# Kernel tuning notes

Measured on AMD Instinct MI355X. Metric: run time of the kernel, lower is better.

The kernel has to match this reference:

```python
import jax, jax.numpy as jnp
import numpy as np

N, E = 10000, 160000
RNA, PROT, EMB, HID, H = 2000, 100, 128, 128, 4
D_IN = 2 * EMB          # 256, input to last block
D_MID = HID * 4         # 512, after conv1/lin1 residual (heads*channel)


def _gat(x, src, dst, Ws, Wd, att_s, att_d, bias, n_nodes, heads):
    # PyG GATConv (tuple in_channels -> separate src/dst linears, concat=True,
    # add_self_loops=False, negative_slope=0.2, eval mode so dropout is identity)
    C = Ws.shape[1] // heads
    xs = (x @ Ws).reshape(n_nodes, heads, C)   # [N,H,C]
    xd = (x @ Wd).reshape(n_nodes, heads, C)
    a_s = jnp.sum(xs * att_s, axis=-1)          # [N,H]
    a_d = jnp.sum(xd * att_d, axis=-1)
    alpha = jax.nn.leaky_relu(a_s[src] + a_d[dst], 0.2)   # [E,H]
    m = jax.ops.segment_max(alpha, dst, num_segments=n_nodes)  # [N,H]
    alpha = jnp.exp(alpha - m[dst])
    denom = jax.ops.segment_sum(alpha, dst, num_segments=n_nodes)
    alpha = alpha / (denom[dst] + 1e-16)
    out = jax.ops.segment_sum(xs[src] * alpha[:, :, None], dst, num_segments=n_nodes)
    return out.reshape(n_nodes, heads * C) + bias


def _layernorm(h, g, b, eps=1e-5):
    mu = jnp.mean(h, axis=-1, keepdims=True)
    var = jnp.mean(jnp.square(h - mu), axis=-1, keepdims=True)
    return (h - mu) * jax.lax.rsqrt(var + eps) * g + b


def setup_inputs() -> dict:
    key = jax.random.key(0)
    ks = iter(jax.random.split(key, 40))
    w = lambda *s: jax.random.normal(next(ks), s, jnp.float32) * 0.02
    z = lambda *s: jnp.zeros(s, jnp.float32)
    inp = {}
    inp["x"] = jax.random.normal(next(ks), (N, RNA + PROT), jnp.float32)
    inp["edge_index"] = jax.random.randint(next(ks), (2, E), 0, N, jnp.int64)
    inp["W_rna"], inp["b_rna"] = w(RNA, EMB), z(EMB)
    inp["W_prot"], inp["b_prot"] = w(PROT, EMB), z(EMB)
    # last GraphAttnBlock (hidden_dim -> hidden_dim), the only one whose output is used
    inp["c1_Ws"], inp["c1_Wd"] = w(D_IN, H * HID), w(D_IN, H * HID)
    inp["c1_as"], inp["c1_ad"] = w(H, HID), w(H, HID)
    inp["c1_b"] = z(H * HID)
    inp["l1_W"], inp["l1_b"] = w(D_IN, D_MID), z(D_MID)
    inp["ln_g"], inp["ln_b"] = jnp.ones((D_MID,), jnp.float32), z(D_MID)
    inp["c2_Ws"], inp["c2_Wd"] = w(D_MID, H * HID), w(D_MID, H * HID)
    inp["c2_as"], inp["c2_ad"] = w(H, HID), w(H, HID)
    inp["c2_b"] = z(H * HID)
    inp["l2_W"], inp["l2_b"] = w(D_MID, D_MID), z(D_MID)
    inp["agg_W"], inp["agg_b"] = w(D_MID, HID), z(HID)
    inp["dr_W"], inp["dr_b"] = w(HID, EMB), z(EMB)
    inp["dp_W"], inp["dp_b"] = w(HID, EMB), z(EMB)
    inp["rr_W"], inp["rr_b"] = w(EMB, RNA), z(RNA)
    inp["rp_W"], inp["rp_b"] = w(EMB, PROT), z(PROT)
    return inp


def reference(x, edge_index, W_rna, b_rna, W_prot, b_prot,
              c1_Ws, c1_Wd, c1_as, c1_ad, c1_b, l1_W, l1_b, ln_g, ln_b,
              c2_Ws, c2_Wd, c2_as, c2_ad, c2_b, l2_W, l2_b,
              agg_W, agg_b, dr_W, dr_b, dp_W, dp_b, rr_W, rr_b, rp_W, rp_b):
    src, dst = edge_index[0], edge_index[1]
    rna_e = x[:, :RNA] @ W_rna + b_rna
    prot_e = x[:, RNA:] @ W_prot + b_prot
    xin = jnp.concatenate([rna_e, prot_e], axis=1)   # raw_x_input [N, 2*EMB]
    # source loops blocks over raw_x_input; only last block output survives
    h = _gat(xin, src, dst, c1_Ws, c1_Wd, c1_as, c1_ad, c1_b, N, H) + (xin @ l1_W + l1_b)
    h = jax.nn.relu(_layernorm(h, ln_g, ln_b))
    h = _gat(h, src, dst, c2_Ws, c2_Wd, c2_as, c2_ad, c2_b, N, H) + (h @ l2_W + l2_b)
    emb = jax.nn.relu(h @ agg_W + agg_b)
    rna_recon = (emb @ dr_W + dr_b) @ rr_W + rr_b
    prot_recon = (emb @ dp_W + dp_b) @ rp_W + rp_b
    return (rna_recon, prot_recon, emb)
```

## Files before the change

### kernel.cpp

```cpp
#include <hip/hip_runtime.h>
#include <hip/hip_bf16.h>
#include <stdint.h>
#include <stddef.h>

using bf16  = __hip_bfloat16;
using bf162 = __hip_bfloat162;

typedef __bf16 bvec8 __attribute__((ext_vector_type(8)));
typedef float  fvec4 __attribute__((ext_vector_type(4)));

struct __align__(16) bf16x8 { bf162 a, b, c, d; };

__device__ __forceinline__ void bf8_to_f(const bf16* p, float* o) {
    bf16x8 v = *reinterpret_cast<const bf16x8*>(p);
    o[0] = __bfloat162float(v.a.x); o[1] = __bfloat162float(v.a.y);
    o[2] = __bfloat162float(v.b.x); o[3] = __bfloat162float(v.b.y);
    o[4] = __bfloat162float(v.c.x); o[5] = __bfloat162float(v.c.y);
    o[6] = __bfloat162float(v.d.x); o[7] = __bfloat162float(v.d.y);
}

__device__ __forceinline__ float wred_sum(float v) {
    #pragma unroll
    for (int o = 32; o > 0; o >>= 1) v += __shfl_xor(v, o);
    return v;
}

__device__ __forceinline__ float wred_max(float v) {
    #pragma unroll
    for (int o = 32; o > 0; o >>= 1) v = fmaxf(v, __shfl_xor(v, o));
    return v;
}

__device__ __forceinline__ float lrelu(float x) { return (x > 0.f) ? x : 0.2f * x; }

__device__ __forceinline__ fvec4 mfma16(bvec8 a, bvec8 b, fvec4 c) {
    return __builtin_amdgcn_mfma_f32_16x16x32_bf16(a, b, c, 0, 0, 0);
}

__device__ __forceinline__ bvec8 ldA(const bf16* p) {
    return *reinterpret_cast<const bvec8*>(p);
}
__device__ __forceinline__ bvec8 ldA(const float* p) {
    float4 f0 = *reinterpret_cast<const float4*>(p);
    float4 f1 = *reinterpret_cast<const float4*>(p + 4);
    union { bvec8 v; bf16 h[8]; } u;
    u.h[0] = __float2bfloat16(f0.x); u.h[1] = __float2bfloat16(f0.y);
    u.h[2] = __float2bfloat16(f0.z); u.h[3] = __float2bfloat16(f0.w);
    u.h[4] = __float2bfloat16(f1.x); u.h[5] = __float2bfloat16(f1.y);
    u.h[6] = __float2bfloat16(f1.z); u.h[7] = __float2bfloat16(f1.w);
    return u.v;
}

__global__ void detect_kernel(const int* __restrict__ ei, int E, int* __restrict__ flags) {
    __shared__ int zc;
    if (threadIdx.x == 0) zc = 0;
    __syncthreads();
    int nodd = E / 2; if (nodd > 1024) nodd = 1024;
    for (int i = threadIdx.x; i < nodd; i += blockDim.x)
        if (ei[2 * i + 1] == 0) atomicAdd(&zc, 1);
    __syncthreads();
    if (threadIdx.x == 0) flags[0] = (zc > nodd / 2) ? 1 : 0;
}

__global__ void conv_edges_kernel(const int* __restrict__ ei, int* __restrict__ src32,
                                  int* __restrict__ dst32, int E, int N,
                                  const int* __restrict__ flags) {
    const int e = blockIdx.x * blockDim.x + threadIdx.x;
    if (e >= E) return;
    int s, d;
    if (flags[0]) { s = ei[2 * e]; d = ei[2 * (E + e)]; }
    else          { s = ei[e];     d = ei[E + e]; }
    src32[e] = (s < 0) ? 0 : ((s >= N) ? N - 1 : s);
    dst32[e] = (d < 0) ? 0 : ((d >= N) ? N - 1 : d);
}

__global__ void zero_int_kernel(int* __restrict__ p, int n) {
    int i = blockIdx.x * blockDim.x + threadIdx.x;
    if (i < n) p[i] = 0;
}

__global__ void hist_kernel(const int* __restrict__ dst32, int* __restrict__ cnt, int E) {
    int e = blockIdx.x * blockDim.x + threadIdx.x;
    if (e < E) atomicAdd(&cnt[dst32[e]], 1);
}

__global__ void scan_kernel(const int* __restrict__ cnt, int* __restrict__ row_ptr, int N) {
    __shared__ int sh[256];
    __shared__ int carry;
    if (threadIdx.x == 0) { carry = 0; row_ptr[0] = 0; }
    __syncthreads();
    for (int base = 0; base < N; base += 256) {
        int i = base + threadIdx.x;
        int v = (i < N) ? cnt[i] : 0;
        sh[threadIdx.x] = v;
        __syncthreads();
        #pragma unroll
        for (int o = 1; o < 256; o <<= 1) {
            int t = (threadIdx.x >= o) ? sh[threadIdx.x - o] : 0;
            __syncthreads();
            sh[threadIdx.x] += t;
            __syncthreads();
        }
        if (i < N) row_ptr[i + 1] = sh[threadIdx.x] + carry;
        __syncthreads();
        if (threadIdx.x == 0) carry += sh[255];
        __syncthreads();
    }
}

__global__ void fill_csr_kernel(const int* __restrict__ src32, const int* __restrict__ dst32,
                                const int* __restrict__ row_ptr, int* __restrict__ cursor,
                                int* __restrict__ col_src, int E) {
    int e = blockIdx.x * blockDim.x + threadIdx.x;
    if (e >= E) return;
    int d = dst32[e];
    int pos = atomicAdd(&cursor[d], 1);
    col_src[row_ptr[d] + pos] = src32[e];
}

__global__ __launch_bounds__(256) void conv_xprot_kernel(const float* __restrict__ x,
                                                         bf16* __restrict__ xp, int N) {
    int idx = blockIdx.x * blockDim.x + threadIdx.x;
    if (idx >= N * 128) return;
    int r = idx >> 7, c = idx & 127;
    float v = (c < 100) ? x[(size_t)r * 2100 + 2000 + c] : 0.f;
    xp[idx] = __float2bfloat16(v);
}

struct WEnt { const float* src; bf16* dst; int K, N, Kp, Np, start; };
struct WTab { WEnt e[12]; int n; };

__global__ __launch_bounds__(256) void wconv_all_kernel(WTab tab) {
    const int b = blockIdx.x;
    int wi = 0;
    #pragma unroll 1
    for (int i = 1; i < tab.n; ++i) if (b >= tab.e[i].start) wi = i;
    const WEnt w = tab.e[wi];
    const int t = (b - w.start) * 256 + threadIdx.x;
    if (t >= w.Np * w.Kp) return;
    const int n = t / w.Kp, k = t - n * w.Kp;
    float v = (n < w.N && k < w.K) ? w.src[(size_t)k * w.N + n] : 0.f;
    w.dst[t] = __float2bfloat16(v);
}

__global__ void bias_fuse_kernel(const float* l1_b, const float* c1_b, float* bsum1,
                                 const float* l2_b, const float* c2_b, float* bsum2,
                                 const float* dr_b, const float* dp_b, float* ddb) {
    int i = blockIdx.x * blockDim.x + threadIdx.x;
    if (i < 512)       bsum1[i] = l1_b[i] + c1_b[i];
    else if (i < 1024) bsum2[i - 512] = l2_b[i - 512] + c2_b[i - 512];
    else if (i < 1152) ddb[i - 1024] = dr_b[i - 1024];
    else if (i < 1280) ddb[i - 1024] = dp_b[i - 1152];
}

template <int FM, bool RELU, typename AT>
__global__ __launch_bounds__(256) void mfma_gemm_kernel(
    const AT* __restrict__ A, int lda,
    const bf16* __restrict__ Bt, int ldb,
    const float* __restrict__ bias,
    float* __restrict__ Cf, int ldcf,
    bf16* __restrict__ Cb, int ldcb,
    int M, int Nn, int K)
{
    const int tid  = threadIdx.x;
    const int w    = tid >> 6, lane = tid & 63;
    const int wr   = w >> 1,   wc   = w & 1;
    const int m0   = blockIdx.y * (FM * 32) + wr * (FM * 16);
    const int n0   = blockIdx.x * 64 + wc * 32;
    const int lrow = lane & 15;
    const int lk8  = (lane >> 4) * 8;

    const AT* Ap[FM];
    #pragma unroll
    for (int i = 0; i < FM; ++i) {
        int r = m0 + i * 16 + lrow;
        if (r > M - 1) r = M - 1;
        Ap[i] = A + (size_t)r * lda + lk8;
    }
    const bf16* Bp = Bt + (size_t)(n0 + lrow) * ldb + lk8;
    const size_t b16 = (size_t)16 * ldb;

    fvec4 acc[FM][2];
    const fvec4 z = {0.f, 0.f, 0.f, 0.f};
    #pragma unroll
    for (int i = 0; i < FM; ++i) { acc[i][0] = z; acc[i][1] = z; }

    #pragma unroll 2
    for (int k = 0; k < K; k += 32) {
        bvec8 b0 = *reinterpret_cast<const bvec8*>(Bp + k);
        bvec8 b1 = *reinterpret_cast<const bvec8*>(Bp + k + b16);
        #pragma unroll
        for (int i = 0; i < FM; ++i) {
            bvec8 a = ldA(Ap[i] + k);
            acc[i][0] = mfma16(a, b0, acc[i][0]);
            acc[i][1] = mfma16(a, b1, acc[i][1]);
        }
    }

    const int r4 = (lane >> 4) * 4;
    #pragma unroll
    for (int fn = 0; fn < 2; ++fn) {
        const int col = n0 + fn * 16 + lrow;
        if (col >= Nn) continue;
        const float bz = bias ? bias[col] : 0.f;
        #pragma unroll
        for (int fm = 0; fm < FM; ++fm) {
            const int rbase = m0 + fm * 16 + r4;
            #pragma unroll
            for (int r = 0; r < 4; ++r) {
                const int row = rbase + r;
                if (row >= M) continue;
                float v = acc[fm][fn][r] + bz;
                if (RELU) v = fmaxf(v, 0.f);
                if (Cf) Cf[(size_t)row * ldcf + col] = v;
                if (Cb) Cb[(size_t)row * ldcb + col] = __float2bfloat16(v);
            }
        }
    }
}

__global__ __launch_bounds__(256) void mfma_gemm_dual_kernel(
    const bf16* __restrict__ A, int lda,
    const bf16* __restrict__ Bt, int ldb,
    const float* __restrict__ biasU,
    bf16* __restrict__ xs, float* __restrict__ hB,
    int M, int K)
{
    const int tid  = threadIdx.x;
    const int w    = tid >> 6, lane = tid & 63;
    const int wr   = w >> 1,   wc   = w & 1;
    const int m0   = blockIdx.y * 128 + wr * 64;
    const int n0   = blockIdx.x * 64 + wc * 32;
    const int lrow = lane & 15;
    const int lk8  = (lane >> 4) * 8;

    const bf16* Ap[4];
    #pragma unroll
    for (int i = 0; i < 4; ++i) {
        int r = m0 + i * 16 + lrow;
        if (r > M - 1) r = M - 1;
        Ap[i] = A + (size_t)r * lda + lk8;
    }
    const bf16* Bp = Bt + (size_t)(n0 + lrow) * ldb + lk8;
    const size_t b16 = (size_t)16 * ldb;

    fvec4 acc[4][2];
    const fvec4 z = {0.f, 0.f, 0.f, 0.f};
    #pragma unroll
    for (int i = 0; i < 4; ++i) { acc[i][0] = z; acc[i][1] = z; }

    #pragma unroll 2
    for (int k = 0; k < K; k += 32) {
        bvec8 b0 = *reinterpret_cast<const bvec8*>(Bp + k);
        bvec8 b1 = *reinterpret_cast<const bvec8*>(Bp + k + b16);
        #pragma unroll
        for (int i = 0; i < 4; ++i) {
            bvec8 a = *reinterpret_cast<const bvec8*>(Ap[i] + k);
            acc[i][0] = mfma16(a, b0, acc[i][0]);
            acc[i][1] = mfma16(a, b1, acc[i][1]);
        }
    }

    const int r4 = (lane >> 4) * 4;
    #pragma unroll
    for (int fn = 0; fn < 2; ++fn) {
        const int col = n0 + fn * 16 + lrow;
        if (col < 512) {
            #pragma unroll
            for (int fm = 0; fm < 4; ++fm) {
                const int rbase = m0 + fm * 16 + r4;
                #pragma unroll
                for (int r = 0; r < 4; ++r) {
                    const int row = rbase + r;
                    if (row >= M) continue;
                    xs[(size_t)row * 512 + col] = __float2bfloat16(acc[fm][fn][r]);
                }
            }
        } else {
            const int c2 = col - 512;
            const float bz = biasU[c2];
            #pragma unroll
            for (int fm = 0; fm < 4; ++fm) {
                const int rbase = m0 + fm * 16 + r4;
                #pragma unroll
                for (int r = 0; r < 4; ++r) {
                    const int row = rbase + r;
                    if (row >= M) continue;
                    hB[(size_t)row * 512 + c2] = acc[fm][fn][r] + bz;
                }
            }
        }
    }
}

__global__ void make_v_kernel(const float* __restrict__ W, const float* __restrict__ att,
                              float* __restrict__ V, int K)
{
    int t = blockIdx.x * blockDim.x + threadIdx.x;
    if (t >= K * 4) return;
    int k = t >> 2, h = t & 3;
    float s = 0.f;
    const float* wp = W + (size_t)k * 512 + h * 128;
    const float* ap = att + h * 128;
    #pragma unroll 4
    for (int c = 0; c < 128; ++c)
        s = fmaf(wp[c], ap[c], s);
    V[k * 4 + h] = s;
}

__global__ __launch_bounds__(64) void logits_kernel(
    const float* __restrict__ X, int ld,
    const float* __restrict__ Vs, const float* __restrict__ Vd,
    float* __restrict__ a_s, float* __restrict__ a_d, int K)
{
    const int n = blockIdx.x, lane = threadIdx.x;
    float ss0=0,ss1=0,ss2=0,ss3=0,dd0=0,dd1=0,dd2=0,dd3=0;
    const float* xr = X + (size_t)n * ld;
    for (int k = lane; k < K; k += 64) {
        float xv = xr[k];
        const float4 vs = *reinterpret_cast<const float4*>(Vs + (size_t)k * 4);
        const float4 vd = *reinterpret_cast<const float4*>(Vd + (size_t)k * 4);
        ss0 = fmaf(xv, vs.x, ss0); ss1 = fmaf(xv, vs.y, ss1);
        ss2 = fmaf(xv, vs.z, ss2); ss3 = fmaf(xv, vs.w, ss3);
        dd0 = fmaf(xv, vd.x, dd0); dd1 = fmaf(xv, vd.y, dd1);
        dd2 = fmaf(xv, vd.z, dd2); dd3 = fmaf(xv, vd.w, dd3);
    }
    ss0 = wred_sum(ss0); ss1 = wred_sum(ss1); ss2 = wred_sum(ss2); ss3 = wred_sum(ss3);
    dd0 = wred_sum(dd0); dd1 = wred_sum(dd1); dd2 = wred_sum(dd2); dd3 = wred_sum(dd3);
    if (lane == 0) {
        a_s[n*4+0]=ss0; a_s[n*4+1]=ss1; a_s[n*4+2]=ss2; a_s[n*4+3]=ss3;
        a_d[n*4+0]=dd0; a_d[n*4+1]=dd1; a_d[n*4+2]=dd2; a_d[n*4+3]=dd3;
    }
}

__global__ __launch_bounds__(64) void gat_gather_kernel(
    const int* __restrict__ row_ptr, const int* __restrict__ col_src,
    const float* __restrict__ a_s, const float* __restrict__ a_d,
    const bf16* __restrict__ xs, float* __restrict__ hout,
    bf16* __restrict__ hout_bf)
{
    const int d = blockIdx.x, lane = threadIdx.x;
    const int beg = row_ptr[d], end = row_ptr[d + 1];
    const float4 ad = *reinterpret_cast<const float4*>(a_d + (size_t)d * 4);

    float m0=-1e30f, m1=-1e30f, m2=-1e30f, m3=-1e30f;
    for (int i = beg + lane; i < end; i += 64) {
        int s = col_src[i];
        float4 as = *reinterpret_cast<const float4*>(a_s + (size_t)s * 4);
        m0 = fmaxf(m0, lrelu(as.x + ad.x));
        m1 = fmaxf(m1, lrelu(as.y + ad.y));
        m2 = fmaxf(m2, lrelu(as.z + ad.z));
        m3 = fmaxf(m3, lrelu(as.w + ad.w));
    }
    m0 = wred_max(m0); m1 = wred_max(m1); m2 = wred_max(m2); m3 = wred_max(m3);

    float d0=0.f, d1=0.f, d2=0.f, d3=0.f;
    for (int i = beg + lane; i < end; i += 64) {
        int s = col_src[i];
        float4 as = *reinterpret_cast<const float4*>(a_s + (size_t)s * 4);
        d0 += __expf(lrelu(as.x + ad.x) - m0);
        d1 += __expf(lrelu(as.y + ad.y) - m1);
        d2 += __expf(lrelu(as.z + ad.z) - m2);
        d3 += __expf(lrelu(as.w + ad.w) - m3);
    }
    d0 = wred_sum(d0); d1 = wred_sum(d1); d2 = wred_sum(d2); d3 = wred_sum(d3);

    const int h = lane >> 4;
    const float mh   = (h == 0) ? m0 : ((h == 1) ? m1 : ((h == 2) ? m2 : m3));
    const float adh  = (h == 0) ? ad.x : ((h == 1) ? ad.y : ((h == 2) ? ad.z : ad.w));
    const float den  = (h == 0) ? d0 : ((h == 1) ? d1 : ((h == 2) ? d2 : d3));
    const float invd = 1.0f / (den + 1e-16f);
    const int c0 = lane * 8;
    float acc[8] = {0.f,0.f,0.f,0.f,0.f,0.f,0.f,0.f};
    for (int i = beg; i < end; ++i) {
        int s = col_src[i];
        float coef = __expf(lrelu(a_s[(size_t)s * 4 + h] + adh) - mh) * invd;
        float xv[8];
        bf8_to_f(xs + (size_t)s * 512 + c0, xv);
        #pragma unroll
        for (int t = 0; t < 8; ++t) acc[t] = fmaf(coef, xv[t], acc[t]);
    }
    float* hp = hout + (size_t)d * 512 + c0;
    if (hout_bf) {
        bf16* hb = hout_bf + (size_t)d * 512 + c0;
        #pragma unroll
        for (int t = 0; t < 8; ++t) {
            float fv = hp[t] + acc[t];
            hp[t] = fv;
            hb[t] = __float2bfloat16(fv);
        }
    } else {
        #pragma unroll
        for (int t = 0; t < 8; ++t) hp[t] += acc[t];
    }
}

__global__ __launch_bounds__(64) void ln_relu_kernel(
    const float* __restrict__ in, const float* __restrict__ g,
    const float* __restrict__ b, float* __restrict__ outp,
    bf16* __restrict__ outbf)
{
    const int n = blockIdx.x, lane = threadIdx.x;
    const int c0 = lane * 8;
    const float* ip = in + (size_t)n * 512 + c0;
    float v[8];
    float4 p0 = *reinterpret_cast<const float4*>(ip);
    float4 p1 = *reinterpret_cast<const float4*>(ip + 4);
    v[0]=p0.x; v[1]=p0.y; v[2]=p0.z; v[3]=p0.w; v[4]=p1.x; v[5]=p1.y; v[6]=p1.z; v[7]=p1.w;
    float s = 0.f;
    #pragma unroll
    for (int t = 0; t < 8; ++t) s += v[t];
    s = wred_sum(s);
    const float mu = s * (1.0f / 512.0f);
    float q = 0.f;
    #pragma unroll
    for (int t = 0; t < 8; ++t) { float dlt = v[t] - mu; q = fmaf(dlt, dlt, q); }
    q = wred_sum(q);
    const float sc = rsqrtf(q * (1.0f / 512.0f) + 1e-5f);
    float4 g0 = *reinterpret_cast<const float4*>(g + c0);
    float4 g1 = *reinterpret_cast<const float4*>(g + c0 + 4);
    float4 b0 = *reinterpret_cast<const float4*>(b + c0);
    float4 b1 = *reinterpret_cast<const float4*>(b + c0 + 4);
    const float gv[8] = {g0.x,g0.y,g0.z,g0.w,g1.x,g1.y,g1.z,g1.w};
    const float bv[8] = {b0.x,b0.y,b0.z,b0.w,b1.x,b1.y,b1.z,b1.w};
    float* op = outp + (size_t)n * 512 + c0;
    bf16*  ob = outbf + (size_t)n * 512 + c0;
    #pragma unroll
    for (int t = 0; t < 8; ++t) {
        float r = fmaxf(0.f, fmaf((v[t] - mu) * sc, gv[t], bv[t]));
        op[t] = r;
        ob[t] = __float2bfloat16(r);
    }
}

extern "C" void kernel_launch(void* const* d_in, const int* in_sizes, int n_in,
                              void* d_out, int out_size, void* d_ws, size_t ws_size,
                              hipStream_t stream)
{
    (void)n_in; (void)out_size; (void)ws_size;
    const float* x   = (const float*)d_in[0];
    const int*   ei  = (const int*)d_in[1];

    const float* W_rna  = (const float*)d_in[2];
    const float* b_rna  = (const float*)d_in[3];
    const float* W_prot = (const float*)d_in[4];
    const float* b_prot = (const float*)d_in[5];
    const float* c1_Ws  = (const float*)d_in[6];
    const float* c1_Wd  = (const float*)d_in[7];
    const float* c1_as  = (const float*)d_in[8];
    const float* c1_ad  = (const float*)d_in[9];
    const float* c1_b   = (const float*)d_in[10];
    const float* l1_W   = (const float*)d_in[11];
    const float* l1_b   = (const float*)d_in[12];
    const float* ln_g   = (const float*)d_in[13];
    const float* ln_b   = (const float*)d_in[14];
    const float* c2_Ws  = (const float*)d_in[15];
    const float* c2_Wd  = (const float*)d_in[16];
    const float* c2_as  = (const float*)d_in[17];
    const float* c2_ad  = (const float*)d_in[18];
    const float* c2_b   = (const float*)d_in[19];
    const float* l2_W   = (const float*)d_in[20];
    const float* l2_b   = (const float*)d_in[21];
    const float* agg_W  = (const float*)d_in[22];
    const float* agg_b  = (const float*)d_in[23];
    const float* dr_W   = (const float*)d_in[24];
    const float* dr_b   = (const float*)d_in[25];
    const float* dp_W   = (const float*)d_in[26];
    const float* dp_b   = (const float*)d_in[27];
    const float* rr_W   = (const float*)d_in[28];
    const float* rr_b   = (const float*)d_in[29];
    const float* rp_W   = (const float*)d_in[30];
    const float* rp_b   = (const float*)d_in[31];

    const int N = in_sizes[0] / 2100;
    const int E = in_sizes[1] / 2;
    const int Mp = ((N + 127) & ~127) + 128;

    char* wsp = (char*)d_ws;
    size_t off = 0;
    auto alloc = [&](size_t bytes) -> void* {
        void* p = wsp + off;
        off += (bytes + 255) & ~(size_t)255;
        return p;
    };
    int*      flags   = (int*)   alloc(16);
    int*      src32   = (int*)   alloc((size_t)E * 4);
    int*      dst32   = (int*)   alloc((size_t)E * 4);
    int*      cnt     = (int*)   alloc((size_t)N * 4);
    int*      cursor  = (int*)   alloc((size_t)N * 4);
    int*      row_ptr = (int*)   alloc((size_t)(N + 1) * 4);
    int*      col_src = (int*)   alloc((size_t)E * 4);
    float*    xin     = (float*) alloc((size_t)N * 256 * 4);
    float*    hA      = (float*) alloc((size_t)N * 512 * 4);
    float*    hB      = (float*) alloc((size_t)N * 512 * 4);
    float*    a_s     = (float*) alloc((size_t)N * 4 * 4);
    float*    a_d     = (float*) alloc((size_t)N * 4 * 4);
    float*    Vs      = (float*) alloc(512 * 4 * 4);
    float*    Vd      = (float*) alloc(512 * 4 * 4);
    float*    bsum1   = (float*) alloc(512 * 4);
    float*    bsum2   = (float*) alloc(512 * 4);
    float*    ddb     = (float*) alloc(256 * 4);
    bf16*     xprot_bf= (bf16*)  alloc((size_t)Mp * 128 * 2);
    bf16*     xin_bf  = (bf16*)  alloc((size_t)Mp * 256 * 2);
    bf16*     hA_bf   = (bf16*)  alloc((size_t)Mp * 512 * 2);
    bf16*     hB_bf   = (bf16*)  alloc((size_t)Mp * 512 * 2);
    bf16*     xs      = (bf16*)  alloc((size_t)Mp * 512 * 2);
    bf16*     emb_bf  = (bf16*)  alloc((size_t)Mp * 128 * 2);
    bf16*     trp     = (bf16*)  alloc((size_t)Mp * 256 * 2);
    bf16*     wrna_t  = (bf16*)  alloc((size_t)128 * 2016 * 2);
    bf16*     wprot_t = (bf16*)  alloc((size_t)128 * 128 * 2);
    bf16*     cb1     = (bf16*)  alloc((size_t)1024 * 256 * 2);
    bf16*     cb2     = (bf16*)  alloc((size_t)1024 * 512 * 2);
    bf16*     aggt    = (bf16*)  alloc((size_t)128 * 512 * 2);
    bf16*     ddt     = (bf16*)  alloc((size_t)256 * 128 * 2);
    bf16*     rrt     = (bf16*)  alloc((size_t)2048 * 128 * 2);
    bf16*     rpt     = (bf16*)  alloc((size_t)128 * 128 * 2);

    const dim3 blk64(64, 1, 1);
    const dim3 blk256(256, 1, 1);
    const dim3 gE((E + 255) / 256);
    const dim3 gN((N + 255) / 256);
    const int GY128 = (N + 127) / 128;
    const int GY64  = (N + 63) / 64;

    float* out0 = (float*)d_out;
    float* out1 = out0 + (size_t)N * 2000;
    float* out2 = out1 + (size_t)N * 100;

    detect_kernel<<<dim3(1), blk256, 0, stream>>>(ei, E, flags);
    conv_edges_kernel<<<gE, blk256, 0, stream>>>(ei, src32, dst32, E, N, flags);
    zero_int_kernel<<<gN, blk256, 0, stream>>>(cnt, N);
    zero_int_kernel<<<gN, blk256, 0, stream>>>(cursor, N);
    hist_kernel<<<gE, blk256, 0, stream>>>(dst32, cnt, E);
    scan_kernel<<<dim3(1), blk256, 0, stream>>>(cnt, row_ptr, N);
    fill_csr_kernel<<<gE, blk256, 0, stream>>>(src32, dst32, row_ptr, cursor, col_src, E);

    {
        WTab tab{};
        int nb = 0, i = 0;
        auto add = [&](const float* s, bf16* d, int K, int Nn, int Kp, int Np) {
            tab.e[i] = {s, d, K, Nn, Kp, Np, nb};
            nb += (Np * Kp + 255) / 256;
            ++i;
        };
        add(W_rna,  wrna_t,          2000, 128, 2016, 128);
        add(W_prot, wprot_t,          100, 128,  128, 128);
        add(c1_Ws,  cb1,              256, 512,  256, 512);
        add(l1_W,   cb1 + 512 * 256,  256, 512,  256, 512);
        add(c2_Ws,  cb2,              512, 512,  512, 512);
        add(l2_W,   cb2 + 512 * 512,  512, 512,  512, 512);
        add(agg_W,  aggt,             512, 128,  512, 128);
        add(dr_W,   ddt,              128, 128,  128, 128);
        add(dp_W,   ddt + 128 * 128,  128, 128,  128, 128);
        add(rr_W,   rrt,              128, 2000, 128, 2048);
        add(rp_W,   rpt,              128, 100,  128, 128);
        tab.n = i;
        wconv_all_kernel<<<dim3(nb), blk256, 0, stream>>>(tab);
    }
    bias_fuse_kernel<<<dim3(5), blk256, 0, stream>>>(l1_b, c1_b, bsum1,
                                                     l2_b, c2_b, bsum2,
                                                     dr_b, dp_b, ddb);
    conv_xprot_kernel<<<dim3((N * 128 + 255) / 256), blk256, 0, stream>>>(x, xprot_bf, N);

    mfma_gemm_kernel<2, false, float><<<dim3(2, GY64), blk256, 0, stream>>>(
        x, 2100, wrna_t, 2016, b_rna, xin, 256, xin_bf, 256, N, 128, 2016);
    mfma_gemm_kernel<2, false, bf16><<<dim3(2, GY64), blk256, 0, stream>>>(
        xprot_bf, 128, wprot_t, 128, b_prot, xin + 128, 256, xin_bf + 128, 256, N, 128, 128);

    make_v_kernel<<<dim3(4), blk256, 0, stream>>>(c1_Ws, c1_as, Vs, 256);
    make_v_kernel<<<dim3(4), blk256, 0, stream>>>(c1_Wd, c1_ad, Vd, 256);
    logits_kernel<<<dim3(N), blk64, 0, stream>>>(xin, 256, Vs, Vd, a_s, a_d, 256);
    mfma_gemm_dual_kernel<<<dim3(16, GY128), blk256, 0, stream>>>(
        xin_bf, 256, cb1, 256, bsum1, xs, hB, N, 256);
    gat_gather_kernel<<<dim3(N), blk64, 0, stream>>>(row_ptr, col_src, a_s, a_d, xs, hB, nullptr);
    ln_relu_kernel<<<dim3(N), blk64, 0, stream>>>(hB, ln_g, ln_b, hA, hA_bf);

    make_v_kernel<<<dim3(8), blk256, 0, stream>>>(c2_Ws, c2_as, Vs, 512);
    make_v_kernel<<<dim3(8), blk256, 0, stream>>>(c2_Wd, c2_ad, Vd, 512);
    logits_kernel<<<dim3(N), blk64, 0, stream>>>(hA, 512, Vs, Vd, a_s, a_d, 512);
    mfma_gemm_dual_kernel<<<dim3(16, GY128), blk256, 0, stream>>>(
        hA_bf, 512, cb2, 512, bsum2, xs, hB, N, 512);
    gat_gather_kernel<<<dim3(N), blk64, 0, stream>>>(row_ptr, col_src, a_s, a_d, xs, hB, hB_bf);

    mfma_gemm_kernel<2, true, bf16><<<dim3(2, GY64), blk256, 0, stream>>>(
        hB_bf, 512, aggt, 512, agg_b, out2, 128, emb_bf, 128, N, 128, 512);
    mfma_gemm_kernel<2, false, bf16><<<dim3(4, GY64), blk256, 0, stream>>>(
        emb_bf, 128, ddt, 128, ddb, nullptr, 0, trp, 256, N, 256, 128);
    mfma_gemm_kernel<4, false, bf16><<<dim3(32, GY128), blk256, 0, stream>>>(
        trp, 256, rrt, 128, rr_b, out0, 2000, nullptr, 0, N, 2000, 128);
    mfma_gemm_kernel<2, false, bf16><<<dim3(2, GY64), blk256, 0, stream>>>(
        trp + 128, 256, rpt, 128, rp_b, out1, 100, nullptr, 0, N, 100, 128);
}
```

Baseline: 683.6 us.

## Fuse embedding GEMMs with split-K, fold logits into reduce and layernorm kernels

The two embedding GEMMs (RNA and protein) become one split-K MFMA GEMM over the full 2100-wide input, using a concatenated block-diagonal transposed weight. This drops the separate protein conversion kernel and uses four K-slices so more blocks run. The partial sums are reduced in a per-node kernel that also adds the bias, writes bf16 output and computes the attention logits, so the fp32 xin buffer and the separate logits passes go away. LayerNorm+ReLU now computes the second-layer logits in the same pass instead of writing an fp32 activation. Smaller launch merges and a gather unroll are also included. The cost is the extra traffic from writing and re-reading the partial-sum buffer.

```diff
diff --git a/kernel.cpp b/kernel.cpp
--- a/kernel.cpp
+++ b/kernel.cpp
@@ -48,6 +48,15 @@
     u.h[2] = __float2bfloat16(f0.z); u.h[3] = __float2bfloat16(f0.w);
     u.h[4] = __float2bfloat16(f1.x); u.h[5] = __float2bfloat16(f1.y);
     u.h[6] = __float2bfloat16(f1.z); u.h[7] = __float2bfloat16(f1.w);
+    return u.v;
+}
+__device__ __forceinline__ bvec8 ldA_mask(const float* p, int kabs) {
+    union { bvec8 v; bf16 h[8]; } u;
+    #pragma unroll
+    for (int j = 0; j < 8; ++j) {
+        float f = (kabs + j < 2100) ? p[j] : 0.f;
+        u.h[j] = __float2bfloat16(f);
+    }
     return u.v;
 }
 
@@ -74,9 +83,9 @@
     dst32[e] = (d < 0) ? 0 : ((d >= N) ? N - 1 : d);
 }
 
-__global__ void zero_int_kernel(int* __restrict__ p, int n) {
+__global__ void zero2_kernel(int* __restrict__ p1, int* __restrict__ p2, int n) {
     int i = blockIdx.x * blockDim.x + threadIdx.x;
-    if (i < n) p[i] = 0;
+    if (i < n) { p1[i] = 0; p2[i] = 0; }
 }
 
 __global__ void hist_kernel(const int* __restrict__ dst32, int* __restrict__ cnt, int E) {
@@ -118,15 +127,6 @@
     col_src[row_ptr[d] + pos] = src32[e];
 }
 
-__global__ __launch_bounds__(256) void conv_xprot_kernel(const float* __restrict__ x,
-                                                         bf16* __restrict__ xp, int N) {
-    int idx = blockIdx.x * blockDim.x + threadIdx.x;
-    if (idx >= N * 128) return;
-    int r = idx >> 7, c = idx & 127;
-    float v = (c < 100) ? x[(size_t)r * 2100 + 2000 + c] : 0.f;
-    xp[idx] = __float2bfloat16(v);
-}
-
 struct WEnt { const float* src; bf16* dst; int K, N, Kp, Np, start; };
 struct WTab { WEnt e[12]; int n; };
 
@@ -143,14 +143,129 @@
     w.dst[t] = __float2bfloat16(v);
 }
 
+__global__ __launch_bounds__(256) void conv_embB_kernel(const float* __restrict__ Wr,
+                                                        const float* __restrict__ Wp,
+                                                        bf16* __restrict__ Bt) {
+    int t = blockIdx.x * 256 + threadIdx.x;
+    if (t >= 256 * 2112) return;
+    int n = t / 2112, k = t - n * 2112;
+    float v = 0.f;
+    if (n < 128) { if (k < 2000) v = Wr[(size_t)k * 128 + n]; }
+    else         { if (k >= 2000 && k < 2100) v = Wp[(size_t)(k - 2000) * 128 + (n - 128)]; }
+    Bt[t] = __float2bfloat16(v);
+}
+
 __global__ void bias_fuse_kernel(const float* l1_b, const float* c1_b, float* bsum1,
                                  const float* l2_b, const float* c2_b, float* bsum2,
-                                 const float* dr_b, const float* dp_b, float* ddb) {
+                                 const float* dr_b, const float* dp_b, float* ddb,
+                                 const float* b_rna, const float* b_prot, float* ebias) {
     int i = blockIdx.x * blockDim.x + threadIdx.x;
     if (i < 512)       bsum1[i] = l1_b[i] + c1_b[i];
     else if (i < 1024) bsum2[i - 512] = l2_b[i - 512] + c2_b[i - 512];
     else if (i < 1152) ddb[i - 1024] = dr_b[i - 1024];
     else if (i < 1280) ddb[i - 1024] = dp_b[i - 1152];
+    else if (i < 1408) ebias[i - 1280] = b_rna[i - 1280];
+    else if (i < 1536) ebias[i - 1280] = b_prot[i - 1408];
+}
+
+__global__ __launch_bounds__(256) void embed_gemm_kernel(
+    const float* __restrict__ x, const bf16* __restrict__ Bt,
+    float* __restrict__ part, int M)
+{
+    const int tid = threadIdx.x;
+    const int w = tid >> 6, lane = tid & 63;
+    const int wr = w >> 1, wc = w & 1;
+    const int m0 = blockIdx.y * 64 + wr * 32;
+    const int n0 = blockIdx.x * 64 + wc * 32;
+    const int z  = blockIdx.z;
+    const int lrow = lane & 15;
+    const int lk8  = (lane >> 4) * 8;
+    const int zp1 = z + 1;
+    const int bs = 32 * (z * 16 + (z < 2 ? z : 2));
+    const int es = 32 * (zp1 * 16 + (zp1 < 2 ? zp1 : 2));
+
+    int r0 = m0 + lrow;      if (r0 > M - 1) r0 = M - 1;
+    int r1 = m0 + 16 + lrow; if (r1 > M - 1) r1 = M - 1;
+    const float* Ap0 = x + (size_t)r0 * 2100 + lk8;
+    const float* Ap1 = x + (size_t)r1 * 2100 + lk8;
+    const bf16*  Bp  = Bt + (size_t)(n0 + lrow) * 2112 + lk8;
+
+    const fvec4 zz = {0.f, 0.f, 0.f, 0.f};
+    fvec4 acc00 = zz, acc01 = zz, acc10 = zz, acc11 = zz;
+
+    for (int k = bs; k < es; k += 32) {
+        bvec8 b0 = *reinterpret_cast<const bvec8*>(Bp + k);
+        bvec8 b1 = *reinterpret_cast<const bvec8*>(Bp + k + 16 * 2112);
+        bvec8 a0, a1;
+        if (k == 2080) {
+            a0 = ldA_mask(Ap0 + k, k + lk8);
+            a1 = ldA_mask(Ap1 + k, k + lk8);
+        } else {
+            a0 = ldA(Ap0 + k);
+            a1 = ldA(Ap1 + k);
+        }
+        acc00 = mfma16(a0, b0, acc00);
+        acc10 = mfma16(a1, b0, acc10);
+        acc01 = mfma16(a0, b1, acc01);
+        acc11 = mfma16(a1, b1, acc11);
+    }
+
+    float* pz = part + (size_t)z * M * 256;
+    const int r4 = (lane >> 4) * 4;
+    #pragma unroll
+    for (int fn = 0; fn < 2; ++fn) {
+        const int col = n0 + fn * 16 + lrow;
+        const fvec4 va = fn ? acc01 : acc00;
+        const fvec4 vb = fn ? acc11 : acc10;
+        #pragma unroll
+        for (int r = 0; r < 4; ++r) {
+            int row0 = m0 + r4 + r;
+            if (row0 < M) pz[(size_t)row0 * 256 + col] = va[r];
+            int row1 = m0 + 16 + r4 + r;
+            if (row1 < M) pz[(size_t)row1 * 256 + col] = vb[r];
+        }
+    }
+}
+
+__global__ __launch_bounds__(64) void embed_reduce_logits_kernel(
+    const float* __restrict__ part, const float* __restrict__ ebias,
+    const float* __restrict__ Vs, const float* __restrict__ Vd,
+    bf16* __restrict__ xin_bf, float* __restrict__ a_s, float* __restrict__ a_d, int M)
+{
+    const int n = blockIdx.x, lane = threadIdx.x;
+    const int c0 = lane * 4;
+    const size_t base = (size_t)n * 256 + c0;
+    float4 v = *reinterpret_cast<const float4*>(part + base);
+    #pragma unroll
+    for (int z = 1; z < 4; ++z) {
+        float4 p = *reinterpret_cast<const float4*>(part + (size_t)z * M * 256 + base);
+        v.x += p.x; v.y += p.y; v.z += p.z; v.w += p.w;
+    }
+    float4 eb = *reinterpret_cast<const float4*>(ebias + c0);
+    v.x += eb.x; v.y += eb.y; v.z += eb.z; v.w += eb.w;
+
+    union { bf16 h[4]; uint2 u; } ob;
+    ob.h[0] = __float2bfloat16(v.x); ob.h[1] = __float2bfloat16(v.y);
+    ob.h[2] = __float2bfloat16(v.z); ob.h[3] = __float2bfloat16(v.w);
+    *reinterpret_cast<uint2*>(xin_bf + base) = ob.u;
+
+    const float vv[4] = {v.x, v.y, v.z, v.w};
+    float ss0=0,ss1=0,ss2=0,ss3=0, dd0=0,dd1=0,dd2=0,dd3=0;
+    #pragma unroll
+    for (int j = 0; j < 4; ++j) {
+        float4 vs = *reinterpret_cast<const float4*>(Vs + (size_t)(c0 + j) * 4);
+        float4 vd = *reinterpret_cast<const float4*>(Vd + (size_t)(c0 + j) * 4);
+        ss0 = fmaf(vv[j], vs.x, ss0); ss1 = fmaf(vv[j], vs.y, ss1);
+        ss2 = fmaf(vv[j], vs.z, ss2); ss3 = fmaf(vv[j], vs.w, ss3);
+        dd0 = fmaf(vv[j], vd.x, dd0); dd1 = fmaf(vv[j], vd.y, dd1);
+        dd2 = fmaf(vv[j], vd.z, dd2); dd3 = fmaf(vv[j], vd.w, dd3);
+    }
+    ss0 = wred_sum(ss0); ss1 = wred_sum(ss1); ss2 = wred_sum(ss2); ss3 = wred_sum(ss3);
+    dd0 = wred_sum(dd0); dd1 = wred_sum(dd1); dd2 = wred_sum(dd2); dd3 = wred_sum(dd3);
+    if (lane == 0) {
+        a_s[n*4+0]=ss0; a_s[n*4+1]=ss1; a_s[n*4+2]=ss2; a_s[n*4+3]=ss3;
+        a_d[n*4+0]=dd0; a_d[n*4+1]=dd1; a_d[n*4+2]=dd2; a_d[n*4+3]=dd3;
+    }
 }
 
 template <int FM, bool RELU, typename AT>
@@ -293,12 +408,19 @@
     }
 }
 
-__global__ void make_v_kernel(const float* __restrict__ W, const float* __restrict__ att,
-                              float* __restrict__ V, int K)
+__global__ void make_v2_kernel(const float* __restrict__ Ws, const float* __restrict__ atts,
+                               float* __restrict__ Vs,
+                               const float* __restrict__ Wd, const float* __restrict__ attd,
+                               float* __restrict__ Vd, int K)
 {
     int t = blockIdx.x * blockDim.x + threadIdx.x;
-    if (t >= K * 4) return;
-    int k = t >> 2, h = t & 3;
+    const int half = K * 4;
+    if (t >= 2 * half) return;
+    const float* W   = (t < half) ? Ws : Wd;
+    const float* att = (t < half) ? atts : attd;
+    float* V         = (t < half) ? Vs : Vd;
+    int tt = (t < half) ? t : t - half;
+    int k = tt >> 2, h = tt & 3;
     float s = 0.f;
     const float* wp = W + (size_t)k * 512 + h * 128;
     const float* ap = att + h * 128;
@@ -306,31 +428,6 @@
     for (int c = 0; c < 128; ++c)
         s = fmaf(wp[c], ap[c], s);
     V[k * 4 + h] = s;
-}
-
-__global__ __launch_bounds__(64) void logits_kernel(
-    const float* __restrict__ X, int ld,
-    const float* __restrict__ Vs, const float* __restrict__ Vd,
-    float* __restrict__ a_s, float* __restrict__ a_d, int K)
-{
-    const int n = blockIdx.x, lane = threadIdx.x;
-    float ss0=0,ss1=0,ss2=0,ss3=0,dd0=0,dd1=0,dd2=0,dd3=0;
-    const float* xr = X + (size_t)n * ld;
-    for (int k = lane; k < K; k += 64) {
-        float xv = xr[k];
-        const float4 vs = *reinterpret_cast<const float4*>(Vs + (size_t)k * 4);
-        const float4 vd = *reinterpret_cast<const float4*>(Vd + (size_t)k * 4);
-        ss0 = fmaf(xv, vs.x, ss0); ss1 = fmaf(xv, vs.y, ss1);
-        ss2 = fmaf(xv, vs.z, ss2); ss3 = fmaf(xv, vs.w, ss3);
-        dd0 = fmaf(xv, vd.x, dd0); dd1 = fmaf(xv, vd.y, dd1);
-        dd2 = fmaf(xv, vd.z, dd2); dd3 = fmaf(xv, vd.w, dd3);
-    }
-    ss0 = wred_sum(ss0); ss1 = wred_sum(ss1); ss2 = wred_sum(ss2); ss3 = wred_sum(ss3);
-    dd0 = wred_sum(dd0); dd1 = wred_sum(dd1); dd2 = wred_sum(dd2); dd3 = wred_sum(dd3);
-    if (lane == 0) {
-        a_s[n*4+0]=ss0; a_s[n*4+1]=ss1; a_s[n*4+2]=ss2; a_s[n*4+3]=ss3;
-        a_d[n*4+0]=dd0; a_d[n*4+1]=dd1; a_d[n*4+2]=dd2; a_d[n*4+3]=dd3;
-    }
 }
 
 __global__ __launch_bounds__(64) void gat_gather_kernel(
@@ -372,6 +469,7 @@
     const float invd = 1.0f / (den + 1e-16f);
     const int c0 = lane * 8;
     float acc[8] = {0.f,0.f,0.f,0.f,0.f,0.f,0.f,0.f};
+    #pragma unroll 2
     for (int i = beg; i < end; ++i) {
         int s = col_src[i];
         float coef = __expf(lrelu(a_s[(size_t)s * 4 + h] + adh) - mh) * invd;
@@ -395,10 +493,11 @@
     }
 }
 
-__global__ __launch_bounds__(64) void ln_relu_kernel(
+__global__ __launch_bounds__(64) void ln_relu_logits_kernel(
     const float* __restrict__ in, const float* __restrict__ g,
-    const float* __restrict__ b, float* __restrict__ outp,
-    bf16* __restrict__ outbf)
+    const float* __restrict__ b,
+    const float* __restrict__ Vs, const float* __restrict__ Vd,
+    bf16* __restrict__ outbf, float* __restrict__ a_s, float* __restrict__ a_d)
 {
     const int n = blockIdx.x, lane = threadIdx.x;
     const int c0 = lane * 8;
@@ -423,13 +522,28 @@
     float4 b1 = *reinterpret_cast<const float4*>(b + c0 + 4);
     const float gv[8] = {g0.x,g0.y,g0.z,g0.w,g1.x,g1.y,g1.z,g1.w};
     const float bv[8] = {b0.x,b0.y,b0.z,b0.w,b1.x,b1.y,b1.z,b1.w};
-    float* op = outp + (size_t)n * 512 + c0;
-    bf16*  ob = outbf + (size_t)n * 512 + c0;
+    float r[8];
+    bf16* ob = outbf + (size_t)n * 512 + c0;
     #pragma unroll
     for (int t = 0; t < 8; ++t) {
-        float r = fmaxf(0.f, fmaf((v[t] - mu) * sc, gv[t], bv[t]));
-        op[t] = r;
-        ob[t] = __float2bfloat16(r);
+        r[t] = fmaxf(0.f, fmaf((v[t] - mu) * sc, gv[t], bv[t]));
+        ob[t] = __float2bfloat16(r[t]);
+    }
+    float ss0=0,ss1=0,ss2=0,ss3=0, dd0=0,dd1=0,dd2=0,dd3=0;
+    #pragma unroll
+    for (int t = 0; t < 8; ++t) {
+        float4 vs = *reinterpret_cast<const float4*>(Vs + (size_t)(c0 + t) * 4);
+        float4 vd = *reinterpret_cast<const float4*>(Vd + (size_t)(c0 + t) * 4);
+        ss0 = fmaf(r[t], vs.x, ss0); ss1 = fmaf(r[t], vs.y, ss1);
+        ss2 = fmaf(r[t], vs.z, ss2); ss3 = fmaf(r[t], vs.w, ss3);
+        dd0 = fmaf(r[t], vd.x, dd0); dd1 = fmaf(r[t], vd.y, dd1);
+        dd2 = fmaf(r[t], vd.z, dd2); dd3 = fmaf(r[t], vd.w, dd3);
+    }
+    ss0 = wred_sum(ss0); ss1 = wred_sum(ss1); ss2 = wred_sum(ss2); ss3 = wred_sum(ss3);
+    dd0 = wred_sum(dd0); dd1 = wred_sum(dd1); dd2 = wred_sum(dd2); dd3 = wred_sum(dd3);
+    if (lane == 0) {
+        a_s[n*4+0]=ss0; a_s[n*4+1]=ss1; a_s[n*4+2]=ss2; a_s[n*4+3]=ss3;
+        a_d[n*4+0]=dd0; a_d[n*4+1]=dd1; a_d[n*4+2]=dd2; a_d[n*4+3]=dd3;
     }
 }
 
@@ -490,8 +604,7 @@
     int*      cursor  = (int*)   alloc((size_t)N * 4);
     int*      row_ptr = (int*)   alloc((size_t)(N + 1) * 4);
     int*      col_src = (int*)   alloc((size_t)E * 4);
-    float*    xin     = (float*) alloc((size_t)N * 256 * 4);
-    float*    hA      = (float*) alloc((size_t)N * 512 * 4);
+    float*    part    = (float*) alloc((size_t)4 * N * 256 * 4);
     float*    hB      = (float*) alloc((size_t)N * 512 * 4);
     float*    a_s     = (float*) alloc((size_t)N * 4 * 4);
     float*    a_d     = (float*) alloc((size_t)N * 4 * 4);
@@ -500,15 +613,14 @@
     float*    bsum1   = (float*) alloc(512 * 4);
     float*    bsum2   = (float*) alloc(512 * 4);
     float*    ddb     = (float*) alloc(256 * 4);
-    bf16*     xprot_bf= (bf16*)  alloc((size_t)Mp * 128 * 2);
+    float*    ebias   = (float*) alloc(256 * 4);
     bf16*     xin_bf  = (bf16*)  alloc((size_t)Mp * 256 * 2);
     bf16*     hA_bf   = (bf16*)  alloc((size_t)Mp * 512 * 2);
     bf16*     hB_bf   = (bf16*)  alloc((size_t)Mp * 512 * 2);
     bf16*     xs      = (bf16*)  alloc((size_t)Mp * 512 * 2);
     bf16*     emb_bf  = (bf16*)  alloc((size_t)Mp * 128 * 2);
     bf16*     trp     = (bf16*)  alloc((size_t)Mp * 256 * 2);
-    bf16*     wrna_t  = (bf16*)  alloc((size_t)128 * 2016 * 2);
-    bf16*     wprot_t = (bf16*)  alloc((size_t)128 * 128 * 2);
+    bf16*     embBt   = (bf16*)  alloc((size_t)256 * 2112 * 2);
     bf16*     cb1     = (bf16*)  alloc((size_t)1024 * 256 * 2);
     bf16*     cb2     = (bf16*)  alloc((size_t)1024 * 512 * 2);
     bf16*     aggt    = (bf16*)  alloc((size_t)128 * 512 * 2);
@@ -529,8 +641,7 @@
 
     detect_kernel<<<dim3(1), blk256, 0, stream>>>(ei, E, flags);
     conv_edges_kernel<<<gE, blk256, 0, stream>>>(ei, src32, dst32, E, N, flags);
-    zero_int_kernel<<<gN, blk256, 0, stream>>>(cnt, N);
-    zero_int_kernel<<<gN, blk256, 0, stream>>>(cursor, N);
+    zero2_kernel<<<gN, blk256, 0, stream>>>(cnt, cursor, N);
     hist_kernel<<<gE, blk256, 0, stream>>>(dst32, cnt, E);
     scan_kernel<<<dim3(1), blk256, 0, stream>>>(cnt, row_ptr, N);
     fill_csr_kernel<<<gE, blk256, 0, stream>>>(src32, dst32, row_ptr, cursor, col_src, E);
@@ -543,8 +654,6 @@
             nb += (Np * Kp + 255) / 256;
             ++i;
         };
-        add(W_rna,  wrna_t,          2000, 128, 2016, 128);
-        add(W_prot, wprot_t,          100, 128,  128, 128);
         add(c1_Ws,  cb1,              256, 512,  256, 512);
         add(l1_W,   cb1 + 512 * 256,  256, 512,  256, 512);
         add(c2_Ws,  cb2,              512, 512,  512, 512);
@@ -557,27 +666,27 @@
         tab.n = i;
         wconv_all_kernel<<<dim3(nb), blk256, 0, stream>>>(tab);
     }
-    bias_fuse_kernel<<<dim3(5), blk256, 0, stream>>>(l1_b, c1_b, bsum1,
+    conv_embB_kernel<<<dim3(256 * 2112 / 256), blk256, 0, stream>>>(W_rna, W_prot, embBt);
+    bias_fuse_kernel<<<dim3(6), blk256, 0, stream>>>(l1_b, c1_b, bsum1,
                                                      l2_b, c2_b, bsum2,
-                                                     dr_b, dp_b, ddb);
-    conv_xprot_kernel<<<dim3((N * 128 + 255) / 256), blk256, 0, stream>>>(x, xprot_bf, N);
-
-    mfma_gemm_kernel<2, false, float><<<dim3(2, GY64), blk256, 0, stream>>>(
-        x, 2100, wrna_t, 2016, b_rna, xin, 256, xin_bf, 256, N, 128, 2016);
-    mfma_gemm_kernel<2, false, bf16><<<dim3(2, GY64), blk256, 0, stream>>>(
-        xprot_bf, 128, wprot_t, 128, b_prot, xin + 128, 256, xin_bf + 128, 256, N, 128, 128);
-
-    make_v_kernel<<<dim3(4), blk256, 0, stream>>>(c1_Ws, c1_as, Vs, 256);
-    make_v_kernel<<<dim3(4), blk256, 0, stream>>>(c1_Wd, c1_ad, Vd, 256);
-    logits_kernel<<<dim3(N), blk64, 0, stream>>>(xin, 256, Vs, Vd, a_s, a_d, 256);
+                                                     dr_b, dp_b, ddb,
+                                                     b_rna, b_prot, ebias);
+    make_v2_kernel<<<dim3((2 * 256 * 4 + 255) / 256), blk256, 0, stream>>>(
+        c1_Ws, c1_as, Vs, c1_Wd, c1_ad, Vd, 256);
+
+    embed_gemm_kernel<<<dim3(4, GY64, 4), blk256, 0, stream>>>(x, embBt, part, N);
+    embed_reduce_logits_kernel<<<dim3(N), blk64, 0, stream>>>(
+        part, ebias, Vs, Vd, xin_bf, a_s, a_d, N);
+
     mfma_gemm_dual_kernel<<<dim3(16, GY128), blk256, 0, stream>>>(
         xin_bf, 256, cb1, 256, bsum1, xs, hB, N, 256);
     gat_gather_kernel<<<dim3(N), blk64, 0, stream>>>(row_ptr, col_src, a_s, a_d, xs, hB, nullptr);
-    ln_relu_kernel<<<dim3(N), blk64, 0, stream>>>(hB, ln_g, ln_b, hA, hA_bf);
-
-    make_v_kernel<<<dim3(8), blk256, 0, stream>>>(c2_Ws, c2_as, Vs, 512);
-    make_v_kernel<<<dim3(8), blk256, 0, stream>>>(c2_Wd, c2_ad, Vd, 512);
-    logits_kernel<<<dim3(N), blk64, 0, stream>>>(hA, 512, Vs, Vd, a_s, a_d, 512);
+
+    make_v2_kernel<<<dim3((2 * 512 * 4 + 255) / 256), blk256, 0, stream>>>(
+        c2_Ws, c2_as, Vs, c2_Wd, c2_ad, Vd, 512);
+    ln_relu_logits_kernel<<<dim3(N), blk64, 0, stream>>>(
+        hB, ln_g, ln_b, Vs, Vd, hA_bf, a_s, a_d);
+
     mfma_gemm_dual_kernel<<<dim3(16, GY128), blk256, 0, stream>>>(
         hA_bf, 512, cb2, 512, bsum2, xs, hB, N, 512);
     gat_gather_kernel<<<dim3(N), blk64, 0, stream>>>(row_ptr, col_src, a_s, a_d, xs, hB, hB_bf);
```

Result: no change. 681.3 us (-0.3%).
